# Performance work log

Hardware: AMD Instinct MI355X
Metric: run time of the kernel (lower is better)

Reference implementation:

```python
import jax, jax.numpy as jnp
import numpy as np

B, N, D, H, O, K, N_USER, C = 1, 4096, 64, 4, 64, 2, 4000, 2


def setup_inputs() -> dict:
    key = jax.random.key(0)
    ks = jax.random.split(key, 7)
    h = jax.random.normal(ks[0], (B, N, D), jnp.float32)
    # dense 0/1 adjacency per heterogeneous kind, with self-loops so no row is empty
    adj = jax.random.randint(ks[1], (K, B, N, N), 0, 2).astype(jnp.float32)
    hadj = jnp.maximum(adj, jnp.eye(N, dtype=jnp.float32))
    s = 1.0 / np.sqrt(D).astype(np.float32)
    w = jax.random.normal(ks[2], (K, H, D, O), jnp.float32) * s
    a_src = jax.random.normal(ks[3], (K, H, O, 1), jnp.float32) * (1.0 / np.sqrt(O).astype(np.float32))
    a_dst = jax.random.normal(ks[4], (K, H, O, 1), jnp.float32) * (1.0 / np.sqrt(O).astype(np.float32))
    fc_w = jax.random.normal(ks[5], (C, O * K), jnp.float32) * (1.0 / np.sqrt(O * K).astype(np.float32))
    fc_b = jnp.zeros((C,), jnp.float32)
    return {"h": h, "hadj": hadj, "w": w, "a_src": a_src, "a_dst": a_dst, "fc_w": fc_w, "fc_b": fc_b}


def _gat(h, adj, w_k, a_src_k, a_dst_k):
    # h: (B,N,D); adj: (B,N,N); w_k: (H,D,O); a_*: (H,O,1)
    h_prime = jnp.einsum('bnf,hfo->bhno', h, w_k)          # (B,H,N,O)
    t = jnp.tanh(h_prime)
    attn_src = jnp.einsum('bhno,hoi->bhni', t, a_src_k)    # (B,H,N,1)
    attn_dst = jnp.einsum('bhno,hoi->bhni', t, a_dst_k)    # (B,H,N,1)
    attn = attn_src + jnp.swapaxes(attn_dst, -1, -2)       # (B,H,N,N) broadcast add
    attn = jnp.where(attn >= 0, attn, 0.2 * attn)          # LeakyReLU(0.2)
    attn = jnp.where(adj[:, None] > 0, attn, -jnp.inf)     # dense mask
    attn = jax.nn.softmax(attn, axis=-1)                   # dropout is a no-op in eval
    out = jnp.einsum('bhnm,bhmo->bhno', attn, h_prime)     # (B,H,N,O)
    return out.mean(axis=1)                                # mean over heads -> (B,N,O)


def reference(h, hadj, w, a_src, a_dst, fc_w, fc_b):
    embs = []
    for k in range(K):  # small fixed loop over heterogeneous node kinds
        x = _gat(h, hadj[k], w[k], a_src[k], a_dst[k])
        embs.append(x[:, :N_USER])
    type_aware = jnp.concatenate(embs, axis=-1)            # (B, N_USER, K*O)
    logits = type_aware @ fc_w.T + fc_b                    # (B, N_USER, C)
    return jax.nn.log_softmax(logits, axis=-1)
```

## Files before the change

kernel.cpp:

```cpp
#include <hip/hip_runtime.h>
#include <math.h>

constexpr int KK = 2;
constexpr int HH = 4;
constexpr int NN = 4096;
constexpr int DD = 64;
constexpr int OO = 64;
constexpr int NU = 4000;
constexpr int CC = 2;
constexpr int JSPLIT = 16;
constexpr int JCHUNK = NN / JSPLIT;
constexpr float LOG2E = 1.44269504088896340736f;

typedef float vf4 __attribute__((ext_vector_type(4)));
typedef float vf2 __attribute__((ext_vector_type(2)));

__device__ __forceinline__ float fexp2(float x) {
#if __has_builtin(__builtin_amdgcn_exp2f)
  return __builtin_amdgcn_exp2f(x);
#else
  return exp2f(x);
#endif
}
__device__ __forceinline__ float frcp(float x) {
#if __has_builtin(__builtin_amdgcn_rcpf)
  return __builtin_amdgcn_rcpf(x);
#else
  return 1.0f / x;
#endif
}
__device__ __forceinline__ float ftanh(float x) {
  float e = fexp2(x * (2.0f * LOG2E));
  return 1.0f - 2.0f * frcp(e + 1.0f);
}

__global__ __launch_bounds__(256) void gat_phase1(
    const float* __restrict__ hsrc, const float* __restrict__ w,
    const float* __restrict__ a_src, const float* __restrict__ a_dst,
    const float* __restrict__ fc_w,
    float* __restrict__ srcAA, float* __restrict__ bb5,
    float* __restrict__ gg) {
  const int kh = blockIdx.y;
  const int k = kh >> 2;
  const int i0 = blockIdx.x * 64;
  const int tid = threadIdx.x;

  __shared__ float h_s[DD][68];
  __shared__ float w_s[DD][OO];
  __shared__ float part[4][64][17];

  {
    const vf4* wp = (const vf4*)(w + (size_t)kh * DD * OO);
    vf4* ws4 = (vf4*)w_s;
    for (int t = tid; t < DD * OO / 4; t += 256) ws4[t] = wp[t];
  }
  for (int t = tid; t < 1024; t += 256) {
    const int row = t >> 4;
    const int f4 = (t & 15) * 4;
    vf4 v = *(const vf4*)(hsrc + (size_t)(i0 + row) * DD + f4);
    h_s[f4 + 0][row] = v.x;
    h_s[f4 + 1][row] = v.y;
    h_s[f4 + 2][row] = v.z;
    h_s[f4 + 3][row] = v.w;
  }
  __syncthreads();

  const int og = tid & 15;
  const int rg = tid >> 4;
  const int o0 = og * 4;
  const int r0 = rg * 4;

  float hp[4][4];
#pragma unroll
  for (int j = 0; j < 4; ++j)
#pragma unroll
    for (int u = 0; u < 4; ++u) hp[j][u] = 0.0f;

#pragma unroll 8
  for (int f = 0; f < DD; ++f) {
    vf4 hv = *(const vf4*)&h_s[f][r0];
    vf4 wv = *(const vf4*)&w_s[f][o0];
    hp[0][0] = fmaf(hv.x, wv.x, hp[0][0]);
    hp[0][1] = fmaf(hv.x, wv.y, hp[0][1]);
    hp[0][2] = fmaf(hv.x, wv.z, hp[0][2]);
    hp[0][3] = fmaf(hv.x, wv.w, hp[0][3]);
    hp[1][0] = fmaf(hv.y, wv.x, hp[1][0]);
    hp[1][1] = fmaf(hv.y, wv.y, hp[1][1]);
    hp[1][2] = fmaf(hv.y, wv.z, hp[1][2]);
    hp[1][3] = fmaf(hv.y, wv.w, hp[1][3]);
    hp[2][0] = fmaf(hv.z, wv.x, hp[2][0]);
    hp[2][1] = fmaf(hv.z, wv.y, hp[2][1]);
    hp[2][2] = fmaf(hv.z, wv.z, hp[2][2]);
    hp[2][3] = fmaf(hv.z, wv.w, hp[2][3]);
    hp[3][0] = fmaf(hv.w, wv.x, hp[3][0]);
    hp[3][1] = fmaf(hv.w, wv.y, hp[3][1]);
    hp[3][2] = fmaf(hv.w, wv.z, hp[3][2]);
    hp[3][3] = fmaf(hv.w, wv.w, hp[3][3]);
  }

  float as[4], ad[4], f0[4], f1[4];
#pragma unroll
  for (int u = 0; u < 4; ++u) {
    as[u] = a_src[kh * OO + o0 + u];
    ad[u] = a_dst[kh * OO + o0 + u];
    f0[u] = fc_w[0 * (KK * OO) + k * OO + o0 + u];
    f1[u] = fc_w[1 * (KK * OO) + k * OO + o0 + u];
  }

#pragma unroll
  for (int j = 0; j < 4; ++j) {
    float sp = 0.0f, dp = 0.0f, g0 = 0.0f, g1 = 0.0f;
#pragma unroll
    for (int u = 0; u < 4; ++u) {
      float v = hp[j][u];
      float t = ftanh(v);
      sp = fmaf(t, as[u], sp);
      dp = fmaf(t, ad[u], dp);
      g0 = fmaf(v, f0[u], g0);
      g1 = fmaf(v, f1[u], g1);
    }
    part[0][r0 + j][og] = sp;
    part[1][r0 + j][og] = dp;
    part[2][r0 + j][og] = g0;
    part[3][r0 + j][og] = g1;
  }
  __syncthreads();

  {
    const int val = tid & 3;
    const int j2 = tid >> 2;
    const float* pr = &part[val][j2][0];
    vf4 s0 = *(const vf4*)(pr + 0);
    vf4 s1 = *(const vf4*)(pr + 4);
    vf4 s2 = *(const vf4*)(pr + 8);
    vf4 s3 = *(const vf4*)(pr + 12);
    vf4 t4 = s0 + s1 + s2 + s3;
    float sum = t4.x + t4.y + t4.z + t4.w;
    const size_t idx = (size_t)kh * NN + i0 + j2;
    if (val == 0) {
      float sp = sum * LOG2E;
      vf2 v = {fexp2(sp), fexp2(0.2f * sp)};
      *(vf2*)(srcAA + idx * 2) = v;
    } else if (val == 1) {
      float dp = sum * LOG2E;
      vf2 v = {fexp2(dp), fexp2(0.2f * dp)};
      *(vf2*)(bb5 + idx * 2) = v;
    } else {
      gg[idx * 2 + (val - 2)] = sum;
    }
  }
}

__global__ __launch_bounds__(256) void gat_phase2(
    const float* __restrict__ adj, const float* __restrict__ srcAA,
    const float* __restrict__ bb5, const float* __restrict__ gg,
    float* __restrict__ P) {
  const int k = blockIdx.y >> 4;
  const int chunk = blockIdx.y & 15;
  const int r0 = blockIdx.x * 16;
  const int tid = threadIdx.x;
  const int wave = tid >> 6;
  const int lane = tid & 63;
  const int row = lane & 15;
  const int jsub = lane >> 4;
  const int i = r0 + row;
  const int j0 = chunk * JCHUNK;

  __shared__ float lds_bb[HH][JCHUNK * 2];
  __shared__ float lds_gg[HH][JCHUNK * 2];

#pragma unroll
  for (int step = 0; step < 4; ++step) {
    const int idx = step * 256 + tid;
    const int sel = idx >> 9;
    const int h = (idx >> 7) & 3;
    const int pos = (idx & 127) * 4;
    const float* src =
        (sel ? gg : bb5) + ((size_t)(k * HH + h) * NN + j0) * 2 + pos;
    vf4 v = *(const vf4*)src;
    if (sel)
      *(vf4*)&lds_gg[h][pos] = v;
    else
      *(vf4*)&lds_bb[h][pos] = v;
  }

  vf2 AA[4];
#pragma unroll
  for (int h = 0; h < 4; ++h)
    AA[h] = *(const vf2*)(srcAA + ((size_t)(k * HH + h) * NN + i) * 2);

  float l[4], a0[4], a1[4];
#pragma unroll
  for (int h = 0; h < 4; ++h) {
    l[h] = 0.0f;
    a0[h] = 0.0f;
    a1[h] = 0.0f;
  }

  __syncthreads();

  const float* arow =
      adj + (size_t)k * NN * NN + (size_t)i * NN + j0 + jsub * 4;
  vf4 aj[4];
#pragma unroll
  for (int q = 0; q < 4; ++q)
    aj[q] = *(const vf4*)(arow + (wave + q * 4) * 16);

#pragma unroll
  for (int s = 0; s < 4; ++s) {
    const int t = wave + s * 4;
    const vf4 av = aj[s];
    const int jl = (t * 16 + jsub * 4) * 2;
#pragma unroll
    for (int h = 0; h < 4; ++h) {
      vf4 b01 = *(const vf4*)&lds_bb[h][jl];
      vf4 b23 = *(const vf4*)&lds_bb[h][jl + 4];
      vf4 g01 = *(const vf4*)&lds_gg[h][jl];
      vf4 g23 = *(const vf4*)&lds_gg[h][jl + 4];
      vf2 bp[4] = {{b01.x, b01.y}, {b01.z, b01.w}, {b23.x, b23.y}, {b23.z, b23.w}};
      vf2 gp[4] = {{g01.x, g01.y}, {g01.z, g01.w}, {g23.x, g23.y}, {g23.z, g23.w}};
#pragma unroll
      for (int jj = 0; jj < 4; ++jj) {
        vf2 PP = AA[h] * bp[jj];
        float e = fmaxf(PP.x, PP.y);
        float pa = e * av[jj];
        l[h] += pa;
        a0[h] = fmaf(pa, gp[jj].x, a0[h]);
        a1[h] = fmaf(pa, gp[jj].y, a1[h]);
      }
    }
  }

#pragma unroll
  for (int h = 0; h < 4; ++h) {
    l[h] += __shfl_xor(l[h], 16, 64);
    l[h] += __shfl_xor(l[h], 32, 64);
    a0[h] += __shfl_xor(a0[h], 16, 64);
    a0[h] += __shfl_xor(a0[h], 32, 64);
    a1[h] += __shfl_xor(a1[h], 16, 64);
    a1[h] += __shfl_xor(a1[h], 32, 64);
  }

  __shared__ float sred[4][12][16];
  if (lane < 16) {
#pragma unroll
    for (int h = 0; h < 4; ++h) {
      sred[wave][h * 3 + 0][row] = l[h];
      sred[wave][h * 3 + 1][row] = a0[h];
      sred[wave][h * 3 + 2][row] = a1[h];
    }
  }
  __syncthreads();
  if (tid < 192) {
    const int v = tid >> 4;
    const int rr = tid & 15;
    float sum =
        sred[0][v][rr] + sred[1][v][rr] + sred[2][v][rr] + sred[3][v][rr];
    const int h = v / 3, c = v % 3;
    size_t base =
        ((((size_t)(k * JSPLIT + chunk) * HH + h) * 3 + c)) * NU + (r0 + rr);
    P[base] = sum;
  }
}

__global__ __launch_bounds__(256) void gat_phase3(
    const float* __restrict__ P, const float* __restrict__ fc_b,
    float* __restrict__ out) {
  const int i = blockIdx.x * 256 + threadIdx.x;
  if (i >= NU) return;
  float l0 = fc_b[0], l1 = fc_b[1];
#pragma unroll
  for (int k = 0; k < KK; ++k) {
#pragma unroll
    for (int q = 0; q < HH; ++q) {
      float ls = 0.0f, a0 = 0.0f, a1 = 0.0f;
#pragma unroll
      for (int ch = 0; ch < JSPLIT; ++ch) {
        size_t b = (((size_t)(k * JSPLIT + ch) * HH + q) * 3) * NU + i;
        ls += P[b];
        a0 += P[b + NU];
        a1 += P[b + 2 * (size_t)NU];
      }
      float inv = 1.0f / ls;
      l0 = fmaf(0.25f * a0, inv, l0);
      l1 = fmaf(0.25f * a1, inv, l1);
    }
  }
  float m = fmaxf(l0, l1);
  float lse = m + logf(expf(l0 - m) + expf(l1 - m));
  out[i * CC + 0] = l0 - lse;
  out[i * CC + 1] = l1 - lse;
}

extern "C" void kernel_launch(void* const* d_in, const int* in_sizes, int n_in,
                              void* d_out, int out_size, void* d_ws, size_t ws_size,
                              hipStream_t stream) {
  const float* hsrc  = (const float*)d_in[0];
  const float* hadj  = (const float*)d_in[1];
  const float* w     = (const float*)d_in[2];
  const float* a_src = (const float*)d_in[3];
  const float* a_dst = (const float*)d_in[4];
  const float* fc_w  = (const float*)d_in[5];
  const float* fc_b  = (const float*)d_in[6];
  float* out = (float*)d_out;

  char* ws = (char*)d_ws;
  float* srcAA = (float*)(ws + 0);
  float* bb5   = (float*)(ws + 262144);
  float* gg    = (float*)(ws + 524288);
  float* P     = (float*)(ws + 786432);

  dim3 g1(NN / 64, KK * HH);
  gat_phase1<<<g1, 256, 0, stream>>>(hsrc, w, a_src, a_dst, fc_w,
                                     srcAA, bb5, gg);
  dim3 g2(NU / 16, KK * JSPLIT);
  gat_phase2<<<g2, 256, 0, stream>>>(hadj, srcAA, bb5, gg, P);
  gat_phase3<<<(NU + 255) / 256, 256, 0, stream>>>(P, fc_b, out);
}
```

Before: 221.8 us.

## Split interleaved pair buffers into planes and parallelize final reduction

Phase 1 now writes the exponentiated source/destination terms and fc projections as separate planar arrays instead of interleaved pairs. Phase 2 loads these planes into LDS and computes with packed two-wide vector math, accumulating in vf2 registers. Phase 3 assigns eight threads per output row (one per kind/head) and reduces with wave shuffles instead of one thread looping over all partials. This aims to cut phase 2 ALU and shuffle overhead and to raise occupancy of the final reduction, at the cost of more global buffers and pointer arguments.

```diff
diff --git a/kernel.cpp b/kernel.cpp
--- a/kernel.cpp
+++ b/kernel.cpp
@@ -38,8 +38,9 @@
     const float* __restrict__ hsrc, const float* __restrict__ w,
     const float* __restrict__ a_src, const float* __restrict__ a_dst,
     const float* __restrict__ fc_w,
-    float* __restrict__ srcAA, float* __restrict__ bb5,
-    float* __restrict__ gg) {
+    float* __restrict__ Ap, float* __restrict__ A5p,
+    float* __restrict__ Bp, float* __restrict__ B5p,
+    float* __restrict__ G0p, float* __restrict__ G1p) {
   const int kh = blockIdx.y;
   const int k = kh >> 2;
   const int i0 = blockIdx.x * 64;
@@ -127,8 +128,8 @@
   __syncthreads();
 
   {
-    const int val = tid & 3;
-    const int j2 = tid >> 2;
+    const int val = tid >> 6;
+    const int j2 = tid & 63;
     const float* pr = &part[val][j2][0];
     vf4 s0 = *(const vf4*)(pr + 0);
     vf4 s1 = *(const vf4*)(pr + 4);
@@ -139,22 +140,25 @@
     const size_t idx = (size_t)kh * NN + i0 + j2;
     if (val == 0) {
       float sp = sum * LOG2E;
-      vf2 v = {fexp2(sp), fexp2(0.2f * sp)};
-      *(vf2*)(srcAA + idx * 2) = v;
+      Ap[idx] = fexp2(sp);
+      A5p[idx] = fexp2(0.2f * sp);
     } else if (val == 1) {
       float dp = sum * LOG2E;
-      vf2 v = {fexp2(dp), fexp2(0.2f * dp)};
-      *(vf2*)(bb5 + idx * 2) = v;
+      Bp[idx] = fexp2(dp);
+      B5p[idx] = fexp2(0.2f * dp);
+    } else if (val == 2) {
+      G0p[idx] = sum;
     } else {
-      gg[idx * 2 + (val - 2)] = sum;
+      G1p[idx] = sum;
     }
   }
 }
 
 __global__ __launch_bounds__(256) void gat_phase2(
-    const float* __restrict__ adj, const float* __restrict__ srcAA,
-    const float* __restrict__ bb5, const float* __restrict__ gg,
-    float* __restrict__ P) {
+    const float* __restrict__ adj, const float* __restrict__ Ap,
+    const float* __restrict__ A5p, const float* __restrict__ Bp,
+    const float* __restrict__ B5p, const float* __restrict__ G0p,
+    const float* __restrict__ G1p, float* __restrict__ P) {
   const int k = blockIdx.y >> 4;
   const int chunk = blockIdx.y & 15;
   const int r0 = blockIdx.x * 16;
@@ -166,35 +170,36 @@
   const int i = r0 + row;
   const int j0 = chunk * JCHUNK;
 
-  __shared__ float lds_bb[HH][JCHUNK * 2];
-  __shared__ float lds_gg[HH][JCHUNK * 2];
-
-#pragma unroll
-  for (int step = 0; step < 4; ++step) {
-    const int idx = step * 256 + tid;
-    const int sel = idx >> 9;
-    const int h = (idx >> 7) & 3;
-    const int pos = (idx & 127) * 4;
-    const float* src =
-        (sel ? gg : bb5) + ((size_t)(k * HH + h) * NN + j0) * 2 + pos;
-    vf4 v = *(const vf4*)src;
-    if (sel)
-      *(vf4*)&lds_gg[h][pos] = v;
-    else
-      *(vf4*)&lds_bb[h][pos] = v;
-  }
-
-  vf2 AA[4];
-#pragma unroll
-  for (int h = 0; h < 4; ++h)
-    AA[h] = *(const vf2*)(srcAA + ((size_t)(k * HH + h) * NN + i) * 2);
-
-  float l[4], a0[4], a1[4];
+  __shared__ float lds[4][HH][JCHUNK];
+
+  {
+    const float* plane_src[4] = {Bp, B5p, G0p, G1p};
+    const int h = tid >> 6;
+    const int pos = (tid & 63) * 4;
+    const size_t gbase = (size_t)(k * HH + h) * NN + j0 + pos;
+#pragma unroll
+    for (int step = 0; step < 4; ++step) {
+      vf4 v = *(const vf4*)(plane_src[step] + gbase);
+      *(vf4*)&lds[step][h][pos] = v;
+    }
+  }
+
+  vf2 Apk[4], A5pk[4];
 #pragma unroll
   for (int h = 0; h < 4; ++h) {
-    l[h] = 0.0f;
-    a0[h] = 0.0f;
-    a1[h] = 0.0f;
+    const size_t ia = (size_t)(k * HH + h) * NN + i;
+    float a = Ap[ia];
+    float a5 = A5p[ia];
+    Apk[h] = (vf2){a, a};
+    A5pk[h] = (vf2){a5, a5};
+  }
+
+  vf2 l2[4], a02[4], a12[4];
+#pragma unroll
+  for (int h = 0; h < 4; ++h) {
+    l2[h] = (vf2){0.0f, 0.0f};
+    a02[h] = (vf2){0.0f, 0.0f};
+    a12[h] = (vf2){0.0f, 0.0f};
   }
 
   __syncthreads();
@@ -210,27 +215,41 @@
   for (int s = 0; s < 4; ++s) {
     const int t = wave + s * 4;
     const vf4 av = aj[s];
-    const int jl = (t * 16 + jsub * 4) * 2;
+    const vf2 av01 = (vf2){av.x, av.y};
+    const vf2 av23 = (vf2){av.z, av.w};
+    const int jl = t * 16 + jsub * 4;
 #pragma unroll
     for (int h = 0; h < 4; ++h) {
-      vf4 b01 = *(const vf4*)&lds_bb[h][jl];
-      vf4 b23 = *(const vf4*)&lds_bb[h][jl + 4];
-      vf4 g01 = *(const vf4*)&lds_gg[h][jl];
-      vf4 g23 = *(const vf4*)&lds_gg[h][jl + 4];
-      vf2 bp[4] = {{b01.x, b01.y}, {b01.z, b01.w}, {b23.x, b23.y}, {b23.z, b23.w}};
-      vf2 gp[4] = {{g01.x, g01.y}, {g01.z, g01.w}, {g23.x, g23.y}, {g23.z, g23.w}};
-#pragma unroll
-      for (int jj = 0; jj < 4; ++jj) {
-        vf2 PP = AA[h] * bp[jj];
-        float e = fmaxf(PP.x, PP.y);
-        float pa = e * av[jj];
-        l[h] += pa;
-        a0[h] = fmaf(pa, gp[jj].x, a0[h]);
-        a1[h] = fmaf(pa, gp[jj].y, a1[h]);
-      }
-    }
-  }
-
+      vf4 Bv = *(const vf4*)&lds[0][h][jl];
+      vf4 B5v = *(const vf4*)&lds[1][h][jl];
+      vf4 G0v = *(const vf4*)&lds[2][h][jl];
+      vf4 G1v = *(const vf4*)&lds[3][h][jl];
+
+      vf2 m01 = Apk[h] * (vf2){Bv.x, Bv.y};
+      vf2 n01 = A5pk[h] * (vf2){B5v.x, B5v.y};
+      vf2 e01 = (vf2){fmaxf(m01.x, n01.x), fmaxf(m01.y, n01.y)};
+      vf2 pa01 = e01 * av01;
+      l2[h] += pa01;
+      a02[h] += pa01 * (vf2){G0v.x, G0v.y};
+      a12[h] += pa01 * (vf2){G1v.x, G1v.y};
+
+      vf2 m23 = Apk[h] * (vf2){Bv.z, Bv.w};
+      vf2 n23 = A5pk[h] * (vf2){B5v.z, B5v.w};
+      vf2 e23 = (vf2){fmaxf(m23.x, n23.x), fmaxf(m23.y, n23.y)};
+      vf2 pa23 = e23 * av23;
+      l2[h] += pa23;
+      a02[h] += pa23 * (vf2){G0v.z, G0v.w};
+      a12[h] += pa23 * (vf2){G1v.z, G1v.w};
+    }
+  }
+
+  float l[4], a0[4], a1[4];
+#pragma unroll
+  for (int h = 0; h < 4; ++h) {
+    l[h] = l2[h].x + l2[h].y;
+    a0[h] = a02[h].x + a02[h].y;
+    a1[h] = a12[h].x + a12[h].y;
+  }
 #pragma unroll
   for (int h = 0; h < 4; ++h) {
     l[h] += __shfl_xor(l[h], 16, 64);
@@ -266,30 +285,39 @@
 __global__ __launch_bounds__(256) void gat_phase3(
     const float* __restrict__ P, const float* __restrict__ fc_b,
     float* __restrict__ out) {
-  const int i = blockIdx.x * 256 + threadIdx.x;
-  if (i >= NU) return;
-  float l0 = fc_b[0], l1 = fc_b[1];
-#pragma unroll
-  for (int k = 0; k < KK; ++k) {
-#pragma unroll
-    for (int q = 0; q < HH; ++q) {
-      float ls = 0.0f, a0 = 0.0f, a1 = 0.0f;
-#pragma unroll
-      for (int ch = 0; ch < JSPLIT; ++ch) {
-        size_t b = (((size_t)(k * JSPLIT + ch) * HH + q) * 3) * NU + i;
-        ls += P[b];
-        a0 += P[b + NU];
-        a1 += P[b + 2 * (size_t)NU];
-      }
-      float inv = 1.0f / ls;
-      l0 = fmaf(0.25f * a0, inv, l0);
-      l1 = fmaf(0.25f * a1, inv, l1);
-    }
-  }
-  float m = fmaxf(l0, l1);
-  float lse = m + logf(expf(l0 - m) + expf(l1 - m));
-  out[i * CC + 0] = l0 - lse;
-  out[i * CC + 1] = l1 - lse;
+  const int tid = threadIdx.x;
+  const int g = tid & 7;
+  const int il = tid >> 3;
+  const int i = blockIdx.x * 32 + il;
+  const int k = g >> 2, h = g & 3;
+
+  float ls = 0.0f, a0 = 0.0f, a1 = 0.0f;
+#pragma unroll
+  for (int ch = 0; ch < JSPLIT; ++ch) {
+    size_t b = (((size_t)(k * JSPLIT + ch) * HH + h) * 3) * NU + i;
+    ls += P[b];
+    a0 += P[b + NU];
+    a1 += P[b + 2 * (size_t)NU];
+  }
+  float inv = 1.0f / ls;
+  float p0 = 0.25f * a0 * inv;
+  float p1 = 0.25f * a1 * inv;
+
+  p0 += __shfl_xor(p0, 1, 64);
+  p0 += __shfl_xor(p0, 2, 64);
+  p0 += __shfl_xor(p0, 4, 64);
+  p1 += __shfl_xor(p1, 1, 64);
+  p1 += __shfl_xor(p1, 2, 64);
+  p1 += __shfl_xor(p1, 4, 64);
+
+  if (g == 0) {
+    float l0 = p0 + fc_b[0];
+    float l1 = p1 + fc_b[1];
+    float m = fmaxf(l0, l1);
+    float lse = m + logf(expf(l0 - m) + expf(l1 - m));
+    out[(size_t)i * CC + 0] = l0 - lse;
+    out[(size_t)i * CC + 1] = l1 - lse;
+  }
 }
 
 extern "C" void kernel_launch(void* const* d_in, const int* in_sizes, int n_in,
@@ -305,15 +333,18 @@
   float* out = (float*)d_out;
 
   char* ws = (char*)d_ws;
-  float* srcAA = (float*)(ws + 0);
-  float* bb5   = (float*)(ws + 262144);
-  float* gg    = (float*)(ws + 524288);
-  float* P     = (float*)(ws + 786432);
+  float* Ap  = (float*)(ws + 0);
+  float* A5p = (float*)(ws + 131072);
+  float* Bp  = (float*)(ws + 262144);
+  float* B5p = (float*)(ws + 393216);
+  float* G0p = (float*)(ws + 524288);
+  float* G1p = (float*)(ws + 655360);
+  float* P   = (float*)(ws + 786432);
 
   dim3 g1(NN / 64, KK * HH);
   gat_phase1<<<g1, 256, 0, stream>>>(hsrc, w, a_src, a_dst, fc_w,
-                                     srcAA, bb5, gg);
+                                     Ap, A5p, Bp, B5p, G0p, G1p);
   dim3 g2(NU / 16, KK * JSPLIT);
-  gat_phase2<<<g2, 256, 0, stream>>>(hadj, srcAA, bb5, gg, P);
-  gat_phase3<<<(NU + 255) / 256, 256, 0, stream>>>(P, fc_b, out);
-}
+  gat_phase2<<<g2, 256, 0, stream>>>(hadj, Ap, A5p, Bp, B5p, G0p, G1p, P);
+  gat_phase3<<<NU / 32, 256, 0, stream>>>(P, fc_b, out);
+}
```

Result: no change. 218.3 us (-1.5%).
